# Kernel tuning notes

Measured on AMD Instinct MI355X. Metric: run time of the kernel, lower is better.

## Reference

```python
import jax, jax.numpy as jnp
import numpy as np

F_DIM = 128


def setup_inputs() -> dict:
    key = jax.random.key(0)
    ks = jax.random.split(key, 10)
    n_atoms = 50000
    n_edges = 500000
    F = F_DIM
    q = jax.random.normal(ks[0], (n_atoms, 1, F), dtype=jnp.float32)
    mu = jax.random.normal(ks[1], (n_atoms, 3, F), dtype=jnp.float32)
    Wij = jax.random.normal(ks[2], (n_edges, 1, 3 * F), dtype=jnp.float32)
    dir_ij = jax.random.normal(ks[3], (n_edges, 3), dtype=jnp.float32)
    idx_i = jax.random.randint(ks[4], (n_edges,), 0, n_atoms, dtype=jnp.int32)
    idx_j = jax.random.randint(ks[5], (n_edges,), 0, n_atoms, dtype=jnp.int32)
    # interatomic_context_net params: Dense(F,F,silu) -> Dense(F,3F)
    s1 = 1.0 / np.sqrt(F)
    W1 = jax.random.uniform(ks[6], (F, F), jnp.float32, -s1, s1)
    b1 = jax.random.uniform(ks[7], (F,), jnp.float32, -s1, s1)
    W2 = jax.random.uniform(ks[8], (F, 3 * F), jnp.float32, -s1, s1)
    b2 = jax.random.uniform(ks[9], (3 * F,), jnp.float32, -s1, s1)
    return {"q": q, "mu": mu, "Wij": Wij, "dir_ij": dir_ij,
            "W1": W1, "b1": b1, "W2": W2, "b2": b2,
            "idx_i": idx_i, "idx_j": idx_j, "n_atoms": n_atoms}


def reference(q, mu, Wij, dir_ij, W1, b1, W2, b2, idx_i, idx_j, n_atoms):
    F = F_DIM
    # context MLP on per-atom scalar features: [n_atoms, 1, 3F]
    h = jax.nn.silu(jnp.einsum('aif,fg->aig', q, W1) + b1)
    x = jnp.einsum('aif,fg->aig', h, W2) + b2
    # gather along edges
    xj = x[idx_j]          # [E, 1, 3F]
    muj = mu[idx_j]        # [E, 3, F]
    xw = Wij * xj          # [E, 1, 3F]
    dq, dmuR, dmumu = jnp.split(xw, 3, axis=-1)  # each [E, 1, F]
    dq_atom = jax.ops.segment_sum(dq, idx_i, num_segments=n_atoms)  # [n_atoms,1,F]
    dmu = dmuR * dir_ij[..., None] + dmumu * muj                    # [E,3,F]
    dmu_atom = jax.ops.segment_sum(dmu, idx_i, num_segments=n_atoms)
    return (q + dq_atom, mu + dmu_atom)
```

## Files before the change

### kernel.cpp

```cpp
#include <hip/hip_runtime.h>

typedef unsigned short u16;
typedef unsigned int   u32;

#define F 128
#define F3 384
#define TA 32
#define PAD 36

__device__ __forceinline__ float bf2f(u16 v) {
    union { u32 u; float f; } c; c.u = ((u32)v) << 16; return c.f;
}
__device__ __forceinline__ u16 f2bf(float f) {
    union { float fv; u32 u; } c; c.fv = f;
    u32 u = c.u;
    return (u16)((u + 0x7fffu + ((u >> 16) & 1u)) >> 16);
}

template<bool BF> __device__ __forceinline__ float LD(const void* p, size_t i) {
    return BF ? bf2f(((const u16*)p)[i]) : ((const float*)p)[i];
}
template<bool BF> __device__ __forceinline__ void ST(void* p, size_t i, float v) {
    if (BF) ((u16*)p)[i] = f2bf(v); else ((float*)p)[i] = v;
}
template<bool BF> __device__ __forceinline__ float2 LD2(const void* p, size_t i) {
    if (BF) {
        u32 v = *(const u32*)((const u16*)p + i);
        float2 r; r.x = bf2f((u16)(v & 0xffff)); r.y = bf2f((u16)(v >> 16)); return r;
    }
    return *(const float2*)((const float*)p + i);
}
template<bool BF> __device__ __forceinline__ void ST2(void* p, size_t i, float2 v) {
    if (BF) { *(u32*)((u16*)p + i) = ((u32)f2bf(v.y) << 16) | f2bf(v.x); }
    else    { *(float2*)((float*)p + i) = v; }
}
__device__ __forceinline__ float2 LD2bf(const u16* p, size_t i) {
    u32 v = *(const u32*)(p + i);
    float2 r; r.x = bf2f((u16)(v & 0xffff)); r.y = bf2f((u16)(v >> 16)); return r;
}
template<bool BF> __device__ __forceinline__ float4 LD4(const void* p, size_t i) {
    if (BF) {
        uint2 v = *(const uint2*)((const u16*)p + i);
        float4 r;
        r.x = bf2f((u16)(v.x & 0xffff)); r.y = bf2f((u16)(v.x >> 16));
        r.z = bf2f((u16)(v.y & 0xffff)); r.w = bf2f((u16)(v.y >> 16));
        return r;
    }
    return *(const float4*)((const float*)p + i);
}

__global__ __launch_bounds__(256) void detect_kernel(const void* q, int* flag) {
    __shared__ int cnt;
    if (threadIdx.x == 0) cnt = 0;
    __syncthreads();
    const u16* p = (const u16*)q;
    int c = 0;
    for (int i = threadIdx.x; i < 1024; i += 256) {
        u16 v = p[2 * i];
        int e = (v >> 7) & 0xFF;
        if (e >= 100 && e <= 150) c++;
    }
    atomicAdd(&cnt, c);
    __syncthreads();
    if (threadIdx.x == 0) *flag = (cnt > 512) ? 1 : 0;
}

template<bool BF>
__device__ void mlp_body(const void* q, const void* W1, const void* b1,
                         const void* W2, const void* b2,
                         u16* __restrict__ xc, u16* __restrict__ hbuf,
                         int cb, int mode, int n_atoms)
{
    __shared__ float qT[F][PAD];
    __shared__ float hT[F][PAD];

    const int tid = threadIdx.x;
    const int a0  = blockIdx.x * TA;
    const int c4  = (tid & 31) * 4;
    const int r4  = (tid >> 5) * 4;

    if (mode == 2) {
        for (int i = tid; i < TA * F / 8; i += 256) {
            int a = i >> 4, f0 = (i & 15) * 8;
            float4 v0, v1;
            if (a0 + a < n_atoms) {
                v0 = LD4<true>(hbuf, (size_t)(a0 + a) * F + f0);
                v1 = LD4<true>(hbuf, (size_t)(a0 + a) * F + f0 + 4);
            } else { v0 = v1 = make_float4(0, 0, 0, 0); }
            hT[f0 + 0][a] = v0.x; hT[f0 + 1][a] = v0.y; hT[f0 + 2][a] = v0.z; hT[f0 + 3][a] = v0.w;
            hT[f0 + 4][a] = v1.x; hT[f0 + 5][a] = v1.y; hT[f0 + 6][a] = v1.z; hT[f0 + 7][a] = v1.w;
        }
        __syncthreads();
    } else {
        for (int i = tid; i < TA * F / 8; i += 256) {
            int a = i >> 4, f0 = (i & 15) * 8;
            float4 v0, v1;
            if (a0 + a < n_atoms) {
                v0 = LD4<BF>(q, (size_t)(a0 + a) * F + f0);
                v1 = LD4<BF>(q, (size_t)(a0 + a) * F + f0 + 4);
            } else { v0 = v1 = make_float4(0, 0, 0, 0); }
            qT[f0 + 0][a] = v0.x; qT[f0 + 1][a] = v0.y; qT[f0 + 2][a] = v0.z; qT[f0 + 3][a] = v0.w;
            qT[f0 + 4][a] = v1.x; qT[f0 + 5][a] = v1.y; qT[f0 + 6][a] = v1.z; qT[f0 + 7][a] = v1.w;
        }
        __syncthreads();

        float acc[4][4];
#pragma unroll
        for (int rr = 0; rr < 4; ++rr)
#pragma unroll
            for (int cc = 0; cc < 4; ++cc) acc[rr][cc] = 0.0f;

        for (int f = 0; f < F; ++f) {
            float4 qv = *(const float4*)&qT[f][r4];
            float4 w  = LD4<BF>(W1, (size_t)f * F + c4);
            float qa[4] = {qv.x, qv.y, qv.z, qv.w};
            float wa[4] = {w.x, w.y, w.z, w.w};
#pragma unroll
            for (int rr = 0; rr < 4; ++rr)
#pragma unroll
                for (int cc = 0; cc < 4; ++cc)
                    acc[rr][cc] += qa[rr] * wa[cc];
        }
        float hv[4][4];
#pragma unroll
        for (int cc = 0; cc < 4; ++cc) {
            float bb = LD<BF>(b1, c4 + cc);
#pragma unroll
            for (int rr = 0; rr < 4; ++rr) {
                float h = acc[rr][cc] + bb;
                float s = h / (1.0f + __expf(-h));
                hv[rr][cc] = s;
                hT[c4 + cc][r4 + rr] = s;
            }
        }
        if (mode == 1) {
#pragma unroll
            for (int rr = 0; rr < 4; ++rr) {
                int ga = a0 + r4 + rr;
                if (ga < n_atoms) {
                    *(u32*)(hbuf + (size_t)ga * F + c4)     = ((u32)f2bf(hv[rr][1]) << 16) | f2bf(hv[rr][0]);
                    *(u32*)(hbuf + (size_t)ga * F + c4 + 2) = ((u32)f2bf(hv[rr][3]) << 16) | f2bf(hv[rr][2]);
                }
            }
        }
        __syncthreads();
    }

    float acc[4][4];
#pragma unroll
    for (int rr = 0; rr < 4; ++rr)
#pragma unroll
        for (int cc = 0; cc < 4; ++cc) acc[rr][cc] = 0.0f;

    for (int f = 0; f < F; ++f) {
        float4 hv = *(const float4*)&hT[f][r4];
        float4 w  = LD4<BF>(W2, (size_t)f * F3 + cb * F + c4);
        float ha[4] = {hv.x, hv.y, hv.z, hv.w};
        float wa[4] = {w.x, w.y, w.z, w.w};
#pragma unroll
        for (int rr = 0; rr < 4; ++rr)
#pragma unroll
            for (int cc = 0; cc < 4; ++cc)
                acc[rr][cc] += ha[rr] * wa[cc];
    }
    float bb[4];
#pragma unroll
    for (int cc = 0; cc < 4; ++cc) bb[cc] = LD<BF>(b2, cb * F + c4 + cc);
#pragma unroll
    for (int rr = 0; rr < 4; ++rr) {
        int ga = a0 + r4 + rr;
        if (ga < n_atoms) {
            float x0 = acc[rr][0] + bb[0], x1 = acc[rr][1] + bb[1];
            float x2 = acc[rr][2] + bb[2], x3 = acc[rr][3] + bb[3];
            *(u32*)(xc + (size_t)ga * F + c4)     = ((u32)f2bf(x1) << 16) | f2bf(x0);
            *(u32*)(xc + (size_t)ga * F + c4 + 2) = ((u32)f2bf(x3) << 16) | f2bf(x2);
        }
    }
}

__global__ __launch_bounds__(256) void mlp_kernel(
    const void* q, const void* W1, const void* b1, const void* W2, const void* b2,
    u16* xc, u16* hbuf, int cb, int mode, int n_atoms, const int* flag)
{
    if (*flag) mlp_body<true >(q, W1, b1, W2, b2, xc, hbuf, cb, mode, n_atoms);
    else       mlp_body<false>(q, W1, b1, W2, b2, xc, hbuf, cb, mode, n_atoms);
}

__global__ __launch_bounds__(256) void count_kernel(
    const int* __restrict__ idx_i, int* __restrict__ counts, int E)
{
    int e = blockIdx.x * 256 + threadIdx.x;
    if (e < E) atomicAdd(&counts[idx_i[e]], 1);
}

__global__ __launch_bounds__(1024) void scan_kernel(
    const int* __restrict__ counts, int* __restrict__ offsets, int n)
{
    __shared__ int buf[1024];
    __shared__ int carryS;
    const int t = threadIdx.x;
    if (t == 0) carryS = 0;
    __syncthreads();

    for (int base = 0; base < n; base += 8192) {
        int idx0 = base + t * 8;
        int c[8];
#pragma unroll
        for (int r = 0; r < 8; ++r) c[r] = (idx0 + r < n) ? counts[idx0 + r] : 0;
        int s = 0;
#pragma unroll
        for (int r = 0; r < 8; ++r) s += c[r];
        buf[t] = s;
        __syncthreads();
        for (int off = 1; off < 1024; off <<= 1) {
            int add = (t >= off) ? buf[t - off] : 0;
            __syncthreads();
            buf[t] += add;
            __syncthreads();
        }
        int run = carryS + buf[t] - s;
#pragma unroll
        for (int r = 0; r < 8; ++r) {
            if (idx0 + r < n) offsets[idx0 + r] = run;
            run += c[r];
        }
        __syncthreads();
        if (t == 0) carryS += buf[1023];
        __syncthreads();
    }
    if (t == 0) offsets[n] = carryS;
}

__global__ __launch_bounds__(256) void scatter_kernel(
    const int* __restrict__ idx_i, const int* __restrict__ offsets,
    int* __restrict__ cursor, int* __restrict__ perm, int E)
{
    int e = blockIdx.x * 256 + threadIdx.x;
    if (e < E) {
        int i = idx_i[e];
        int pos = offsets[i] + atomicAdd(&cursor[i], 1);
        perm[pos] = e;
    }
}

template<bool BF>
__device__ void gq_body(const void* q, const void* Wij, const u16* __restrict__ xc,
                        const int* __restrict__ idx_j, const int* __restrict__ offsets,
                        const int* __restrict__ perm, void* out, int n_atoms, int E)
{
    int a    = blockIdx.x * 4 + (threadIdx.x >> 6);
    int lane = threadIdx.x & 63;
    if (a >= n_atoms) return;
    const size_t fo = 2 * lane;

    float2 s = LD2<BF>(q, (size_t)a * F + fo);
    int k0 = offsets[a], k1 = offsets[a + 1];
    for (int kb = k0; kb < k1; kb += 64) {
        int cnt = k1 - kb; if (cnt > 64) cnt = 64;
        int e_r = 0, j_r = 0;
        if (lane < cnt) {
            e_r = perm[kb + lane]; if ((unsigned)e_r >= (unsigned)E) e_r = 0;
            j_r = idx_j[e_r];      if ((unsigned)j_r >= (unsigned)n_atoms) j_r = 0;
        }
        for (int c = 0; c < cnt; ++c) {
            int e = __shfl(e_r, c, 64);
            int j = __shfl(j_r, c, 64);
            float2 w  = LD2<BF>(Wij, (size_t)e * F3 + fo);
            float2 xv = LD2bf(xc, (size_t)j * F + fo);
            s.x += w.x * xv.x;
            s.y += w.y * xv.y;
        }
    }
    ST2<BF>(out, (size_t)a * F + fo, s);
}

__global__ __launch_bounds__(256) void gather_q_kernel(
    const void* q, const void* Wij, const u16* xc, const int* idx_j,
    const int* offsets, const int* perm, void* out, int n_atoms, int E, const int* flag)
{
    if (*flag) gq_body<true >(q, Wij, xc, idx_j, offsets, perm, out, n_atoms, E);
    else       gq_body<false>(q, Wij, xc, idx_j, offsets, perm, out, n_atoms, E);
}

template<bool BF, int MODE>
__device__ void gmu_body(const void* mu, const void* Wij, const void* dir,
                         const u16* __restrict__ xc, const int* __restrict__ idx_j,
                         const int* __restrict__ offsets, const int* __restrict__ perm,
                         void* out, int n_atoms, int E)
{
    int a    = blockIdx.x * 4 + (threadIdx.x >> 6);
    int lane = threadIdx.x & 63;
    if (a >= n_atoms) return;
    const size_t fo = 2 * lane;
    const size_t ob = (size_t)n_atoms * F;

    float2 s0, s1, s2;
    if (MODE == 1) {
        s0 = LD2<BF>(mu, (size_t)a * F3 + fo);
        s1 = LD2<BF>(mu, (size_t)a * F3 + 128 + fo);
        s2 = LD2<BF>(mu, (size_t)a * F3 + 256 + fo);
    } else {
        s0 = LD2<BF>(out, ob + (size_t)a * F3 + fo);
        s1 = LD2<BF>(out, ob + (size_t)a * F3 + 128 + fo);
        s2 = LD2<BF>(out, ob + (size_t)a * F3 + 256 + fo);
    }

    const int wofs = (MODE == 1) ? 128 : 256;
    int k0 = offsets[a], k1 = offsets[a + 1];
    for (int kb = k0; kb < k1; kb += 64) {
        int cnt = k1 - kb; if (cnt > 64) cnt = 64;
        int e_r = 0, j_r = 0;
        if (lane < cnt) {
            e_r = perm[kb + lane]; if ((unsigned)e_r >= (unsigned)E) e_r = 0;
            j_r = idx_j[e_r];      if ((unsigned)j_r >= (unsigned)n_atoms) j_r = 0;
        }
        for (int c = 0; c < cnt; ++c) {
            int e = __shfl(e_r, c, 64);
            int j = __shfl(j_r, c, 64);
            float2 w  = LD2<BF>(Wij, (size_t)e * F3 + wofs + fo);
            float2 xv = LD2bf(xc, (size_t)j * F + fo);
            float wx0 = w.x * xv.x, wx1 = w.y * xv.y;
            if (MODE == 1) {
                float d0 = LD<BF>(dir, (size_t)e * 3 + 0);
                float d1 = LD<BF>(dir, (size_t)e * 3 + 1);
                float d2 = LD<BF>(dir, (size_t)e * 3 + 2);
                s0.x += wx0 * d0; s0.y += wx1 * d0;
                s1.x += wx0 * d1; s1.y += wx1 * d1;
                s2.x += wx0 * d2; s2.y += wx1 * d2;
            } else {
                float2 m0 = LD2<BF>(mu, (size_t)j * F3 + fo);
                float2 m1 = LD2<BF>(mu, (size_t)j * F3 + 128 + fo);
                float2 m2 = LD2<BF>(mu, (size_t)j * F3 + 256 + fo);
                s0.x += wx0 * m0.x; s0.y += wx1 * m0.y;
                s1.x += wx0 * m1.x; s1.y += wx1 * m1.y;
                s2.x += wx0 * m2.x; s2.y += wx1 * m2.y;
            }
        }
    }
    ST2<BF>(out, ob + (size_t)a * F3 + fo,       s0);
    ST2<BF>(out, ob + (size_t)a * F3 + 128 + fo, s1);
    ST2<BF>(out, ob + (size_t)a * F3 + 256 + fo, s2);
}

__global__ __launch_bounds__(256) void gather_mu_kernel(
    const void* mu, const void* Wij, const void* dir, const u16* xc,
    const int* idx_j, const int* offsets, const int* perm, void* out,
    int n_atoms, int E, int mode, const int* flag)
{
    if (*flag) {
        if (mode == 1) gmu_body<true, 1>(mu, Wij, dir, xc, idx_j, offsets, perm, out, n_atoms, E);
        else           gmu_body<true, 2>(mu, Wij, dir, xc, idx_j, offsets, perm, out, n_atoms, E);
    } else {
        if (mode == 1) gmu_body<false, 1>(mu, Wij, dir, xc, idx_j, offsets, perm, out, n_atoms, E);
        else           gmu_body<false, 2>(mu, Wij, dir, xc, idx_j, offsets, perm, out, n_atoms, E);
    }
}

extern "C" void kernel_launch(void* const* d_in, const int* in_sizes, int n_in,
                              void* d_out, int out_size, void* d_ws, size_t ws_size,
                              hipStream_t stream)
{
    const void* q   = d_in[0];
    const void* mu  = d_in[1];
    const void* Wij = d_in[2];
    const void* dir = d_in[3];
    const void* W1  = d_in[4];
    const void* b1  = d_in[5];
    const void* W2  = d_in[6];
    const void* b2  = d_in[7];
    const int* idx_i = (const int*)d_in[8];
    const int* idx_j = (const int*)d_in[9];

    const int n_atoms = in_sizes[0] / F;
    const int E       = in_sizes[8];

    u16* xc      = (u16*)d_ws;
    int* flag    = (int*)(xc + (size_t)n_atoms * F);
    int* counts  = flag + 4;
    int* cursor  = counts + n_atoms;
    int* offsets = cursor + n_atoms;
    int* perm    = offsets + n_atoms + 1;
    u16* hbuf    = (u16*)(perm + E);
    size_t need_h = (size_t)((char*)(hbuf + (size_t)n_atoms * F) - (char*)d_ws);
    const bool useH = (ws_size >= need_h);

    detect_kernel<<<1, 256, 0, stream>>>(q, flag);

    hipMemsetAsync(counts, 0, (size_t)2 * n_atoms * sizeof(int), stream);
    int eBlocks = (E + 255) / 256;
    count_kernel<<<eBlocks, 256, 0, stream>>>(idx_i, counts, E);
    scan_kernel<<<1, 1024, 0, stream>>>(counts, offsets, n_atoms);
    scatter_kernel<<<eBlocks, 256, 0, stream>>>(idx_i, offsets, cursor, perm, E);

    int mlpBlocks = (n_atoms + TA - 1) / TA;
    int gBlocks   = (n_atoms + 3) / 4;

    mlp_kernel<<<mlpBlocks, 256, 0, stream>>>(q, W1, b1, W2, b2, xc, hbuf, 0,
                                              useH ? 1 : 0, n_atoms, flag);
    gather_q_kernel<<<gBlocks, 256, 0, stream>>>(q, Wij, xc, idx_j, offsets, perm,
                                                 d_out, n_atoms, E, flag);
    mlp_kernel<<<mlpBlocks, 256, 0, stream>>>(q, W1, b1, W2, b2, xc, hbuf, 1,
                                              useH ? 2 : 0, n_atoms, flag);
    gather_mu_kernel<<<gBlocks, 256, 0, stream>>>(mu, Wij, dir, xc, idx_j, offsets, perm,
                                                  d_out, n_atoms, E, 1, flag);
    mlp_kernel<<<mlpBlocks, 256, 0, stream>>>(q, W1, b1, W2, b2, xc, hbuf, 2,
                                              useH ? 2 : 0, n_atoms, flag);
    gather_mu_kernel<<<gBlocks, 256, 0, stream>>>(mu, Wij, dir, xc, idx_j, offsets, perm,
                                                  d_out, n_atoms, E, 2, flag);
}
```

Measured before the change: 682.0 us.

## Fuse MLP into one pass and merge q/mu gathers into one edge kernel

Adds a path, used when the workspace is large enough, that computes all three output chunks of the context MLP in one kernel into a full bf16 x buffer. It converts mu to bf16 once, then runs a single CSR gather kernel that accumulates dq and all three dmu components per edge. This replaces three MLP launches and three gather passes that each re-read the edge indices, Wij and neighbour rows. The scan kernel is also reworked to a single pass with per-thread contiguous chunks. The trade-off is a larger workspace, lower mu precision from the bf16 copy, and more registers in the fused gather.

```diff
diff --git a/kernel.cpp b/kernel.cpp
--- a/kernel.cpp
+++ b/kernel.cpp
@@ -63,6 +63,125 @@
     atomicAdd(&cnt, c);
     __syncthreads();
     if (threadIdx.x == 0) *flag = (cnt > 512) ? 1 : 0;
+}
+
+template<bool BF>
+__device__ void convmu_body(const void* mu, u16* dst, size_t n) {
+    size_t i = ((size_t)blockIdx.x * 256 + threadIdx.x) * 8;
+    if (i >= n) return;
+    if (BF) {
+        *(uint4*)(dst + i) = *(const uint4*)((const u16*)mu + i);
+    } else {
+        float4 a = *(const float4*)((const float*)mu + i);
+        float4 b = *(const float4*)((const float*)mu + i + 4);
+        uint4 o;
+        o.x = ((u32)f2bf(a.y) << 16) | f2bf(a.x);
+        o.y = ((u32)f2bf(a.w) << 16) | f2bf(a.z);
+        o.z = ((u32)f2bf(b.y) << 16) | f2bf(b.x);
+        o.w = ((u32)f2bf(b.w) << 16) | f2bf(b.z);
+        *(uint4*)(dst + i) = o;
+    }
+}
+__global__ __launch_bounds__(256) void convmu_kernel(const void* mu, u16* dst,
+                                                     size_t n, const int* flag) {
+    if (*flag) convmu_body<true >(mu, dst, n);
+    else       convmu_body<false>(mu, dst, n);
+}
+
+template<bool BF>
+__device__ void mlpfull_body(const void* q, const void* W1, const void* b1,
+                             const void* W2, const void* b2,
+                             u16* __restrict__ xcf, int n_atoms)
+{
+    __shared__ float qT[F][PAD];
+    __shared__ float hT[F][PAD];
+
+    const int tid = threadIdx.x;
+    const int a0  = blockIdx.x * TA;
+    const int c4  = (tid & 31) * 4;
+    const int r4  = (tid >> 5) * 4;
+
+    for (int i = tid; i < TA * F / 8; i += 256) {
+        int a = i >> 4, f0 = (i & 15) * 8;
+        float4 v0, v1;
+        if (a0 + a < n_atoms) {
+            v0 = LD4<BF>(q, (size_t)(a0 + a) * F + f0);
+            v1 = LD4<BF>(q, (size_t)(a0 + a) * F + f0 + 4);
+        } else { v0 = v1 = make_float4(0, 0, 0, 0); }
+        qT[f0 + 0][a] = v0.x; qT[f0 + 1][a] = v0.y; qT[f0 + 2][a] = v0.z; qT[f0 + 3][a] = v0.w;
+        qT[f0 + 4][a] = v1.x; qT[f0 + 5][a] = v1.y; qT[f0 + 6][a] = v1.z; qT[f0 + 7][a] = v1.w;
+    }
+    __syncthreads();
+
+    {
+        float acc[4][4];
+#pragma unroll
+        for (int rr = 0; rr < 4; ++rr)
+#pragma unroll
+            for (int cc = 0; cc < 4; ++cc) acc[rr][cc] = 0.0f;
+
+        for (int f = 0; f < F; ++f) {
+            float4 qv = *(const float4*)&qT[f][r4];
+            float4 w  = LD4<BF>(W1, (size_t)f * F + c4);
+            float qa[4] = {qv.x, qv.y, qv.z, qv.w};
+            float wa[4] = {w.x, w.y, w.z, w.w};
+#pragma unroll
+            for (int rr = 0; rr < 4; ++rr)
+#pragma unroll
+                for (int cc = 0; cc < 4; ++cc)
+                    acc[rr][cc] += qa[rr] * wa[cc];
+        }
+#pragma unroll
+        for (int cc = 0; cc < 4; ++cc) {
+            float bb = LD<BF>(b1, c4 + cc);
+#pragma unroll
+            for (int rr = 0; rr < 4; ++rr) {
+                float h = acc[rr][cc] + bb;
+                hT[c4 + cc][r4 + rr] = h / (1.0f + __expf(-h));
+            }
+        }
+    }
+    __syncthreads();
+
+    for (int cb = 0; cb < 3; ++cb) {
+        float acc[4][4];
+#pragma unroll
+        for (int rr = 0; rr < 4; ++rr)
+#pragma unroll
+            for (int cc = 0; cc < 4; ++cc) acc[rr][cc] = 0.0f;
+
+        for (int f = 0; f < F; ++f) {
+            float4 hv = *(const float4*)&hT[f][r4];
+            float4 w  = LD4<BF>(W2, (size_t)f * F3 + cb * F + c4);
+            float ha[4] = {hv.x, hv.y, hv.z, hv.w};
+            float wa[4] = {w.x, w.y, w.z, w.w};
+#pragma unroll
+            for (int rr = 0; rr < 4; ++rr)
+#pragma unroll
+                for (int cc = 0; cc < 4; ++cc)
+                    acc[rr][cc] += ha[rr] * wa[cc];
+        }
+        float bb[4];
+#pragma unroll
+        for (int cc = 0; cc < 4; ++cc) bb[cc] = LD<BF>(b2, cb * F + c4 + cc);
+#pragma unroll
+        for (int rr = 0; rr < 4; ++rr) {
+            int ga = a0 + r4 + rr;
+            if (ga < n_atoms) {
+                uint2 o;
+                o.x = ((u32)f2bf(acc[rr][1] + bb[1]) << 16) | f2bf(acc[rr][0] + bb[0]);
+                o.y = ((u32)f2bf(acc[rr][3] + bb[3]) << 16) | f2bf(acc[rr][2] + bb[2]);
+                *(uint2*)(xcf + (size_t)ga * F3 + cb * F + c4) = o;
+            }
+        }
+    }
+}
+__global__ __launch_bounds__(256) void mlpfull_kernel(
+    const void* q, const void* W1, const void* b1, const void* W2, const void* b2,
+    u16* xcf, int n_atoms, const int* flag)
+{
+    if (*flag) mlpfull_body<true >(q, W1, b1, W2, b2, xcf, n_atoms);
+    else       mlpfull_body<false>(q, W1, b1, W2, b2, xcf, n_atoms);
 }
 
 template<bool BF>
@@ -170,14 +289,11 @@
     for (int rr = 0; rr < 4; ++rr) {
         int ga = a0 + r4 + rr;
         if (ga < n_atoms) {
-            float x0 = acc[rr][0] + bb[0], x1 = acc[rr][1] + bb[1];
-            float x2 = acc[rr][2] + bb[2], x3 = acc[rr][3] + bb[3];
-            *(u32*)(xc + (size_t)ga * F + c4)     = ((u32)f2bf(x1) << 16) | f2bf(x0);
-            *(u32*)(xc + (size_t)ga * F + c4 + 2) = ((u32)f2bf(x3) << 16) | f2bf(x2);
-        }
-    }
-}
-
+            *(u32*)(xc + (size_t)ga * F + c4)     = ((u32)f2bf(acc[rr][1] + bb[1]) << 16) | f2bf(acc[rr][0] + bb[0]);
+            *(u32*)(xc + (size_t)ga * F + c4 + 2) = ((u32)f2bf(acc[rr][3] + bb[3]) << 16) | f2bf(acc[rr][2] + bb[2]);
+        }
+    }
+}
 __global__ __launch_bounds__(256) void mlp_kernel(
     const void* q, const void* W1, const void* b1, const void* W2, const void* b2,
     u16* xc, u16* hbuf, int cb, int mode, int n_atoms, const int* flag)
@@ -197,38 +313,28 @@
     const int* __restrict__ counts, int* __restrict__ offsets, int n)
 {
     __shared__ int buf[1024];
-    __shared__ int carryS;
     const int t = threadIdx.x;
-    if (t == 0) carryS = 0;
+    const int m = (n + 1023) >> 10;
+    const int i0 = t * m;
+    int s = 0;
+    for (int r = 0; r < m; ++r) {
+        int i = i0 + r;
+        if (i < n) s += counts[i];
+    }
+    buf[t] = s;
     __syncthreads();
-
-    for (int base = 0; base < n; base += 8192) {
-        int idx0 = base + t * 8;
-        int c[8];
-#pragma unroll
-        for (int r = 0; r < 8; ++r) c[r] = (idx0 + r < n) ? counts[idx0 + r] : 0;
-        int s = 0;
-#pragma unroll
-        for (int r = 0; r < 8; ++r) s += c[r];
-        buf[t] = s;
+    for (int off = 1; off < 1024; off <<= 1) {
+        int add = (t >= off) ? buf[t - off] : 0;
         __syncthreads();
-        for (int off = 1; off < 1024; off <<= 1) {
-            int add = (t >= off) ? buf[t - off] : 0;
-            __syncthreads();
-            buf[t] += add;
-            __syncthreads();
-        }
-        int run = carryS + buf[t] - s;
-#pragma unroll
-        for (int r = 0; r < 8; ++r) {
-            if (idx0 + r < n) offsets[idx0 + r] = run;
-            run += c[r];
-        }
+        buf[t] += add;
         __syncthreads();
-        if (t == 0) carryS += buf[1023];
-        __syncthreads();
-    }
-    if (t == 0) offsets[n] = carryS;
+    }
+    int run = buf[t] - s;
+    for (int r = 0; r < m; ++r) {
+        int i = i0 + r;
+        if (i < n) { offsets[i] = run; run += counts[i]; }
+    }
+    if (t == 1023) offsets[n] = buf[1023];
 }
 
 __global__ __launch_bounds__(256) void scatter_kernel(
@@ -241,6 +347,75 @@
         int pos = offsets[i] + atomicAdd(&cursor[i], 1);
         perm[pos] = e;
     }
+}
+
+template<bool BF>
+__device__ void gfused_body(const void* q, const void* mu, const void* Wij,
+                            const void* dir, const u16* __restrict__ xcf,
+                            const u16* __restrict__ mubf,
+                            const int* __restrict__ idx_j,
+                            const int* __restrict__ offsets,
+                            const int* __restrict__ perm,
+                            void* out, int n_atoms, int E)
+{
+    int a    = blockIdx.x * 4 + (threadIdx.x >> 6);
+    int lane = threadIdx.x & 63;
+    if (a >= n_atoms) return;
+    const size_t fo = 2 * lane;
+    const size_t ob = (size_t)n_atoms * F;
+
+    float2 sq = LD2<BF>(q, (size_t)a * F + fo);
+    float2 s0 = LD2<BF>(mu, (size_t)a * F3 + fo);
+    float2 s1 = LD2<BF>(mu, (size_t)a * F3 + 128 + fo);
+    float2 s2 = LD2<BF>(mu, (size_t)a * F3 + 256 + fo);
+
+    int k0 = offsets[a], k1 = offsets[a + 1];
+    for (int kb = k0; kb < k1; kb += 64) {
+        int cnt = k1 - kb; if (cnt > 64) cnt = 64;
+        int e_r = 0, j_r = 0;
+        if (lane < cnt) {
+            e_r = perm[kb + lane]; if ((unsigned)e_r >= (unsigned)E) e_r = 0;
+            j_r = idx_j[e_r];      if ((unsigned)j_r >= (unsigned)n_atoms) j_r = 0;
+        }
+#pragma unroll 2
+        for (int c = 0; c < cnt; ++c) {
+            int e = __shfl(e_r, c, 64);
+            int j = __shfl(j_r, c, 64);
+            const size_t wb = (size_t)e * F3;
+            const size_t jb = (size_t)j * F3;
+            float2 wq = LD2<BF>(Wij, wb + fo);
+            float2 wR = LD2<BF>(Wij, wb + 128 + fo);
+            float2 wm = LD2<BF>(Wij, wb + 256 + fo);
+            float2 xq = LD2bf(xcf, jb + fo);
+            float2 xR = LD2bf(xcf, jb + 128 + fo);
+            float2 xm = LD2bf(xcf, jb + 256 + fo);
+            float2 m0 = LD2bf(mubf, jb + fo);
+            float2 m1 = LD2bf(mubf, jb + 128 + fo);
+            float2 m2 = LD2bf(mubf, jb + 256 + fo);
+            float d0 = LD<BF>(dir, (size_t)e * 3 + 0);
+            float d1 = LD<BF>(dir, (size_t)e * 3 + 1);
+            float d2 = LD<BF>(dir, (size_t)e * 3 + 2);
+
+            sq.x += wq.x * xq.x;           sq.y += wq.y * xq.y;
+            float tR0 = wR.x * xR.x,  tR1 = wR.y * xR.y;
+            float tm0 = wm.x * xm.x,  tm1 = wm.y * xm.y;
+            s0.x += tR0 * d0 + tm0 * m0.x; s0.y += tR1 * d0 + tm1 * m0.y;
+            s1.x += tR0 * d1 + tm0 * m1.x; s1.y += tR1 * d1 + tm1 * m1.y;
+            s2.x += tR0 * d2 + tm0 * m2.x; s2.y += tR1 * d2 + tm1 * m2.y;
+        }
+    }
+    ST2<BF>(out, (size_t)a * F + fo, sq);
+    ST2<BF>(out, ob + (size_t)a * F3 + fo,       s0);
+    ST2<BF>(out, ob + (size_t)a * F3 + 128 + fo, s1);
+    ST2<BF>(out, ob + (size_t)a * F3 + 256 + fo, s2);
+}
+__global__ __launch_bounds__(256) void gfused_kernel(
+    const void* q, const void* mu, const void* Wij, const void* dir,
+    const u16* xcf, const u16* mubf, const int* idx_j, const int* offsets,
+    const int* perm, void* out, int n_atoms, int E, const int* flag)
+{
+    if (*flag) gfused_body<true >(q, mu, Wij, dir, xcf, mubf, idx_j, offsets, perm, out, n_atoms, E);
+    else       gfused_body<false>(q, mu, Wij, dir, xcf, mubf, idx_j, offsets, perm, out, n_atoms, E);
 }
 
 template<bool BF>
@@ -273,7 +448,6 @@
     }
     ST2<BF>(out, (size_t)a * F + fo, s);
 }
-
 __global__ __launch_bounds__(256) void gather_q_kernel(
     const void* q, const void* Wij, const u16* xc, const int* idx_j,
     const int* offsets, const int* perm, void* out, int n_atoms, int E, const int* flag)
@@ -341,7 +515,6 @@
     ST2<BF>(out, ob + (size_t)a * F3 + 128 + fo, s1);
     ST2<BF>(out, ob + (size_t)a * F3 + 256 + fo, s2);
 }
-
 __global__ __launch_bounds__(256) void gather_mu_kernel(
     const void* mu, const void* Wij, const void* dir, const u16* xc,
     const int* idx_j, const int* offsets, const int* perm, void* out,
@@ -373,6 +546,37 @@
 
     const int n_atoms = in_sizes[0] / F;
     const int E       = in_sizes[8];
+    const int eBlocks = (E + 255) / 256;
+    const int gBlocks = (n_atoms + 3) / 4;
+    const int mlpBlocks = (n_atoms + TA - 1) / TA;
+
+    {
+        u16* xcf     = (u16*)d_ws;
+        u16* mubf    = xcf + (size_t)n_atoms * F3;
+        int* flag    = (int*)(mubf + (size_t)n_atoms * F3);
+        int* counts  = flag + 4;
+        int* cursor  = counts + n_atoms;
+        int* offsets = cursor + n_atoms;
+        int* perm    = offsets + n_atoms + 1;
+        size_t need  = (size_t)((char*)(perm + E) - (char*)d_ws);
+
+        if (ws_size >= need) {
+            detect_kernel<<<1, 256, 0, stream>>>(q, flag);
+            hipMemsetAsync(counts, 0, (size_t)2 * n_atoms * sizeof(int), stream);
+            count_kernel<<<eBlocks, 256, 0, stream>>>(idx_i, counts, E);
+            scan_kernel<<<1, 1024, 0, stream>>>(counts, offsets, n_atoms);
+            scatter_kernel<<<eBlocks, 256, 0, stream>>>(idx_i, offsets, cursor, perm, E);
+
+            size_t nmu = (size_t)n_atoms * F3;
+            convmu_kernel<<<(int)((nmu / 8 + 255) / 256), 256, 0, stream>>>(mu, mubf, nmu, flag);
+            mlpfull_kernel<<<mlpBlocks, 256, 0, stream>>>(q, W1, b1, W2, b2, xcf, n_atoms, flag);
+
+            gfused_kernel<<<gBlocks, 256, 0, stream>>>(q, mu, Wij, dir, xcf, mubf,
+                                                       idx_j, offsets, perm, d_out,
+                                                       n_atoms, E, flag);
+            return;
+        }
+    }
 
     u16* xc      = (u16*)d_ws;
     int* flag    = (int*)(xc + (size_t)n_atoms * F);
@@ -385,15 +589,10 @@
     const bool useH = (ws_size >= need_h);
 
     detect_kernel<<<1, 256, 0, stream>>>(q, flag);
-
     hipMemsetAsync(counts, 0, (size_t)2 * n_atoms * sizeof(int), stream);
-    int eBlocks = (E + 255) / 256;
     count_kernel<<<eBlocks, 256, 0, stream>>>(idx_i, counts, E);
     scan_kernel<<<1, 1024, 0, stream>>>(counts, offsets, n_atoms);
     scatter_kernel<<<eBlocks, 256, 0, stream>>>(idx_i, offsets, cursor, perm, E);
-
-    int mlpBlocks = (n_atoms + TA - 1) / TA;
-    int gBlocks   = (n_atoms + 3) / 4;
 
     mlp_kernel<<<mlpBlocks, 256, 0, stream>>>(q, W1, b1, W2, b2, xc, hbuf, 0,
                                               useH ? 1 : 0, n_atoms, flag);
```

Result: faster. 605.0 us (-11.3%).

## Fuse three gather passes into one with interleaved per-atom x/mu rows

Applied to the files above, without the earlier changes.

Replaces the three separate MLP+gather passes with a single MLP kernel that computes all three 128-wide output chunks and one fused gather kernel that reads each edge's full Wij row once. The x values and a bf16 copy of mu are interleaved into one 768-element row per atom, so each neighbor needs one contiguous fetch. The sorted edge list is packed into int4 records carrying e, j and bf16 direction, and Wij loads and output stores use nontemporal hints. This cuts repeated reads of Wij, idx_j and mu along with extra launches. In exchange it uses a larger workspace, quantizes mu and dir to bf16 in the gather, and keeps more registers live in the MLP.

```diff
diff --git a/kernel.cpp b/kernel.cpp
--- a/kernel.cpp
+++ b/kernel.cpp
@@ -2,11 +2,13 @@
 
 typedef unsigned short u16;
 typedef unsigned int   u32;
+typedef unsigned long long u64;
 
 #define F 128
 #define F3 384
 #define TA 32
 #define PAD 36
+#define ROW 768
 
 __device__ __forceinline__ float bf2f(u16 v) {
     union { u32 u; float f; } c; c.u = ((u32)v) << 16; return c.f;
@@ -16,12 +18,18 @@
     u32 u = c.u;
     return (u16)((u + 0x7fffu + ((u >> 16) & 1u)) >> 16);
 }
+__device__ __forceinline__ float u2f(u32 v) {
+    union { u32 u; float f; } c; c.u = v; return c.f;
+}
+__device__ __forceinline__ u32 f2u(float v) {
+    union { float f; u32 u; } c; c.f = v; return c.u;
+}
+__device__ __forceinline__ u32 pk(float a, float b) {
+    return ((u32)f2bf(b) << 16) | f2bf(a);
+}
 
 template<bool BF> __device__ __forceinline__ float LD(const void* p, size_t i) {
     return BF ? bf2f(((const u16*)p)[i]) : ((const float*)p)[i];
-}
-template<bool BF> __device__ __forceinline__ void ST(void* p, size_t i, float v) {
-    if (BF) ((u16*)p)[i] = f2bf(v); else ((float*)p)[i] = v;
 }
 template<bool BF> __device__ __forceinline__ float2 LD2(const void* p, size_t i) {
     if (BF) {
@@ -31,7 +39,7 @@
     return *(const float2*)((const float*)p + i);
 }
 template<bool BF> __device__ __forceinline__ void ST2(void* p, size_t i, float2 v) {
-    if (BF) { *(u32*)((u16*)p + i) = ((u32)f2bf(v.y) << 16) | f2bf(v.x); }
+    if (BF) { *(u32*)((u16*)p + i) = pk(v.x, v.y); }
     else    { *(float2*)((float*)p + i) = v; }
 }
 __device__ __forceinline__ float2 LD2bf(const u16* p, size_t i) {
@@ -48,6 +56,24 @@
     }
     return *(const float4*)((const float*)p + i);
 }
+template<bool BF> __device__ __forceinline__ float2 NTLD2(const void* p, size_t i) {
+    if (BF) {
+        u32 v = __builtin_nontemporal_load((const u32*)((const u16*)p + i));
+        float2 r; r.x = bf2f((u16)(v & 0xffff)); r.y = bf2f((u16)(v >> 16)); return r;
+    } else {
+        u64 v = __builtin_nontemporal_load((const u64*)((const float*)p + i));
+        float2 r; r.x = u2f((u32)v); r.y = u2f((u32)(v >> 32)); return r;
+    }
+}
+template<bool BF> __device__ __forceinline__ void NTST2(void* p, size_t i, float2 v) {
+    if (BF) {
+        u32 o = pk(v.x, v.y);
+        __builtin_nontemporal_store(o, (u32*)((u16*)p + i));
+    } else {
+        u64 o = ((u64)f2u(v.y) << 32) | f2u(v.x);
+        __builtin_nontemporal_store(o, (u64*)((float*)p + i));
+    }
+}
 
 __global__ __launch_bounds__(256) void detect_kernel(const void* q, int* flag) {
     __shared__ int cnt;
@@ -66,10 +92,27 @@
 }
 
 template<bool BF>
-__device__ void mlp_body(const void* q, const void* W1, const void* b1,
-                         const void* W2, const void* b2,
-                         u16* __restrict__ xc, u16* __restrict__ hbuf,
-                         int cb, int mode, int n_atoms)
+__device__ void mu12_body(const void* mu, u16* xm12, int n_atoms) {
+    int a = blockIdx.x * 4 + (threadIdx.x >> 6);
+    int p = threadIdx.x & 63;
+    if (a >= n_atoms) return;
+    float2 m0 = LD2<BF>(mu, (size_t)a * F3 + 2 * p);
+    float2 m1 = LD2<BF>(mu, (size_t)a * F3 + 128 + 2 * p);
+    float2 m2 = LD2<BF>(mu, (size_t)a * F3 + 256 + 2 * p);
+    u16* base = xm12 + (size_t)a * ROW + p * 12;
+    *(u32*)(base + 6) = pk(m0.x, m0.y);
+    *(uint2*)(base + 8) = make_uint2(pk(m1.x, m1.y), pk(m2.x, m2.y));
+}
+__global__ __launch_bounds__(256) void mu12_kernel(const void* mu, u16* xm12,
+                                                   int n_atoms, const int* flag) {
+    if (*flag) mu12_body<true >(mu, xm12, n_atoms);
+    else       mu12_body<false>(mu, xm12, n_atoms);
+}
+
+template<bool BF>
+__device__ void mlpfull_body(const void* q, const void* W1, const void* b1,
+                             const void* W2, const void* b2,
+                             u16* __restrict__ xm12, int n_atoms)
 {
     __shared__ float qT[F][PAD];
     __shared__ float hT[F][PAD];
@@ -79,31 +122,19 @@
     const int c4  = (tid & 31) * 4;
     const int r4  = (tid >> 5) * 4;
 
-    if (mode == 2) {
-        for (int i = tid; i < TA * F / 8; i += 256) {
-            int a = i >> 4, f0 = (i & 15) * 8;
-            float4 v0, v1;
-            if (a0 + a < n_atoms) {
-                v0 = LD4<true>(hbuf, (size_t)(a0 + a) * F + f0);
-                v1 = LD4<true>(hbuf, (size_t)(a0 + a) * F + f0 + 4);
-            } else { v0 = v1 = make_float4(0, 0, 0, 0); }
-            hT[f0 + 0][a] = v0.x; hT[f0 + 1][a] = v0.y; hT[f0 + 2][a] = v0.z; hT[f0 + 3][a] = v0.w;
-            hT[f0 + 4][a] = v1.x; hT[f0 + 5][a] = v1.y; hT[f0 + 6][a] = v1.z; hT[f0 + 7][a] = v1.w;
-        }
-        __syncthreads();
-    } else {
-        for (int i = tid; i < TA * F / 8; i += 256) {
-            int a = i >> 4, f0 = (i & 15) * 8;
-            float4 v0, v1;
-            if (a0 + a < n_atoms) {
-                v0 = LD4<BF>(q, (size_t)(a0 + a) * F + f0);
-                v1 = LD4<BF>(q, (size_t)(a0 + a) * F + f0 + 4);
-            } else { v0 = v1 = make_float4(0, 0, 0, 0); }
-            qT[f0 + 0][a] = v0.x; qT[f0 + 1][a] = v0.y; qT[f0 + 2][a] = v0.z; qT[f0 + 3][a] = v0.w;
-            qT[f0 + 4][a] = v1.x; qT[f0 + 5][a] = v1.y; qT[f0 + 6][a] = v1.z; qT[f0 + 7][a] = v1.w;
-        }
-        __syncthreads();
-
+    for (int i = tid; i < TA * F / 8; i += 256) {
+        int a = i >> 4, f0 = (i & 15) * 8;
+        float4 v0, v1;
+        if (a0 + a < n_atoms) {
+            v0 = LD4<BF>(q, (size_t)(a0 + a) * F + f0);
+            v1 = LD4<BF>(q, (size_t)(a0 + a) * F + f0 + 4);
+        } else { v0 = v1 = make_float4(0, 0, 0, 0); }
+        qT[f0 + 0][a] = v0.x; qT[f0 + 1][a] = v0.y; qT[f0 + 2][a] = v0.z; qT[f0 + 3][a] = v0.w;
+        qT[f0 + 4][a] = v1.x; qT[f0 + 5][a] = v1.y; qT[f0 + 6][a] = v1.z; qT[f0 + 7][a] = v1.w;
+    }
+    __syncthreads();
+
+    {
         float acc[4][4];
 #pragma unroll
         for (int rr = 0; rr < 4; ++rr)
@@ -121,69 +152,68 @@
                 for (int cc = 0; cc < 4; ++cc)
                     acc[rr][cc] += qa[rr] * wa[cc];
         }
-        float hv[4][4];
 #pragma unroll
         for (int cc = 0; cc < 4; ++cc) {
             float bb = LD<BF>(b1, c4 + cc);
 #pragma unroll
             for (int rr = 0; rr < 4; ++rr) {
                 float h = acc[rr][cc] + bb;
-                float s = h / (1.0f + __expf(-h));
-                hv[rr][cc] = s;
-                hT[c4 + cc][r4 + rr] = s;
+                hT[c4 + cc][r4 + rr] = h / (1.0f + __expf(-h));
             }
         }
-        if (mode == 1) {
-#pragma unroll
-            for (int rr = 0; rr < 4; ++rr) {
-                int ga = a0 + r4 + rr;
-                if (ga < n_atoms) {
-                    *(u32*)(hbuf + (size_t)ga * F + c4)     = ((u32)f2bf(hv[rr][1]) << 16) | f2bf(hv[rr][0]);
-                    *(u32*)(hbuf + (size_t)ga * F + c4 + 2) = ((u32)f2bf(hv[rr][3]) << 16) | f2bf(hv[rr][2]);
-                }
-            }
-        }
-        __syncthreads();
-    }
-
-    float acc[4][4];
-#pragma unroll
-    for (int rr = 0; rr < 4; ++rr)
-#pragma unroll
-        for (int cc = 0; cc < 4; ++cc) acc[rr][cc] = 0.0f;
-
-    for (int f = 0; f < F; ++f) {
-        float4 hv = *(const float4*)&hT[f][r4];
-        float4 w  = LD4<BF>(W2, (size_t)f * F3 + cb * F + c4);
-        float ha[4] = {hv.x, hv.y, hv.z, hv.w};
-        float wa[4] = {w.x, w.y, w.z, w.w};
+    }
+    __syncthreads();
+
+    float xout[4][4][3];
+#pragma unroll
+    for (int cb = 0; cb < 3; ++cb) {
+        float acc[4][4];
 #pragma unroll
         for (int rr = 0; rr < 4; ++rr)
 #pragma unroll
-            for (int cc = 0; cc < 4; ++cc)
-                acc[rr][cc] += ha[rr] * wa[cc];
-    }
-    float bb[4];
-#pragma unroll
-    for (int cc = 0; cc < 4; ++cc) bb[cc] = LD<BF>(b2, cb * F + c4 + cc);
+            for (int cc = 0; cc < 4; ++cc) acc[rr][cc] = 0.0f;
+
+        for (int f = 0; f < F; ++f) {
+            float4 hv = *(const float4*)&hT[f][r4];
+            float4 w  = LD4<BF>(W2, (size_t)f * F3 + cb * F + c4);
+            float ha[4] = {hv.x, hv.y, hv.z, hv.w};
+            float wa[4] = {w.x, w.y, w.z, w.w};
+#pragma unroll
+            for (int rr = 0; rr < 4; ++rr)
+#pragma unroll
+                for (int cc = 0; cc < 4; ++cc)
+                    acc[rr][cc] += ha[rr] * wa[cc];
+        }
+#pragma unroll
+        for (int cc = 0; cc < 4; ++cc) {
+            float bb = LD<BF>(b2, cb * F + c4 + cc);
+#pragma unroll
+            for (int rr = 0; rr < 4; ++rr)
+                xout[rr][cc][cb] = acc[rr][cc] + bb;
+        }
+    }
 #pragma unroll
     for (int rr = 0; rr < 4; ++rr) {
         int ga = a0 + r4 + rr;
         if (ga < n_atoms) {
-            float x0 = acc[rr][0] + bb[0], x1 = acc[rr][1] + bb[1];
-            float x2 = acc[rr][2] + bb[2], x3 = acc[rr][3] + bb[3];
-            *(u32*)(xc + (size_t)ga * F + c4)     = ((u32)f2bf(x1) << 16) | f2bf(x0);
-            *(u32*)(xc + (size_t)ga * F + c4 + 2) = ((u32)f2bf(x3) << 16) | f2bf(x2);
-        }
-    }
-}
-
-__global__ __launch_bounds__(256) void mlp_kernel(
+            int p0 = c4 >> 1;
+            u16* b0 = xm12 + (size_t)ga * ROW + p0 * 12;
+            *(uint2*)(b0) = make_uint2(pk(xout[rr][0][0], xout[rr][1][0]),
+                                       pk(xout[rr][0][1], xout[rr][1][1]));
+            *(u32*)(b0 + 4) = pk(xout[rr][0][2], xout[rr][1][2]);
+            u16* b1p = b0 + 12;
+            *(uint2*)(b1p) = make_uint2(pk(xout[rr][2][0], xout[rr][3][0]),
+                                        pk(xout[rr][2][1], xout[rr][3][1]));
+            *(u32*)(b1p + 4) = pk(xout[rr][2][2], xout[rr][3][2]);
+        }
+    }
+}
+__global__ __launch_bounds__(256) void mlpfull_kernel(
     const void* q, const void* W1, const void* b1, const void* W2, const void* b2,
-    u16* xc, u16* hbuf, int cb, int mode, int n_atoms, const int* flag)
-{
-    if (*flag) mlp_body<true >(q, W1, b1, W2, b2, xc, hbuf, cb, mode, n_atoms);
-    else       mlp_body<false>(q, W1, b1, W2, b2, xc, hbuf, cb, mode, n_atoms);
+    u16* xm12, int n_atoms, const int* flag)
+{
+    if (*flag) mlpfull_body<true >(q, W1, b1, W2, b2, xm12, n_atoms);
+    else       mlpfull_body<false>(q, W1, b1, W2, b2, xm12, n_atoms);
 }
 
 __global__ __launch_bounds__(256) void count_kernel(
@@ -197,96 +227,64 @@
     const int* __restrict__ counts, int* __restrict__ offsets, int n)
 {
     __shared__ int buf[1024];
-    __shared__ int carryS;
     const int t = threadIdx.x;
-    if (t == 0) carryS = 0;
-    __syncthreads();
-
-    for (int base = 0; base < n; base += 8192) {
-        int idx0 = base + t * 8;
-        int c[8];
-#pragma unroll
-        for (int r = 0; r < 8; ++r) c[r] = (idx0 + r < n) ? counts[idx0 + r] : 0;
-        int s = 0;
-#pragma unroll
-        for (int r = 0; r < 8; ++r) s += c[r];
-        buf[t] = s;
+    const int m = (n + 1023) >> 10;
+    const int i0 = t * m;
+    int s = 0;
+    for (int r = 0; r < m; ++r) {
+        int i = i0 + r;
+        if (i < n) s += counts[i];
+    }
+    buf[t] = s;
+    __syncthreads();
+    for (int off = 1; off < 1024; off <<= 1) {
+        int add = (t >= off) ? buf[t - off] : 0;
         __syncthreads();
-        for (int off = 1; off < 1024; off <<= 1) {
-            int add = (t >= off) ? buf[t - off] : 0;
-            __syncthreads();
-            buf[t] += add;
-            __syncthreads();
-        }
-        int run = carryS + buf[t] - s;
-#pragma unroll
-        for (int r = 0; r < 8; ++r) {
-            if (idx0 + r < n) offsets[idx0 + r] = run;
-            run += c[r];
-        }
+        buf[t] += add;
         __syncthreads();
-        if (t == 0) carryS += buf[1023];
-        __syncthreads();
-    }
-    if (t == 0) offsets[n] = carryS;
-}
-
-__global__ __launch_bounds__(256) void scatter_kernel(
-    const int* __restrict__ idx_i, const int* __restrict__ offsets,
-    int* __restrict__ cursor, int* __restrict__ perm, int E)
+    }
+    int run = buf[t] - s;
+    for (int r = 0; r < m; ++r) {
+        int i = i0 + r;
+        if (i < n) { offsets[i] = run; run += counts[i]; }
+    }
+    if (t == 1023) offsets[n] = buf[1023];
+}
+
+template<bool BF>
+__device__ void scatter_body(const int* __restrict__ idx_i, const int* __restrict__ idx_j,
+                             const void* __restrict__ dir, const int* __restrict__ offsets,
+                             int* __restrict__ cursor, int4* __restrict__ ej4, int E)
 {
     int e = blockIdx.x * 256 + threadIdx.x;
     if (e < E) {
         int i = idx_i[e];
         int pos = offsets[i] + atomicAdd(&cursor[i], 1);
-        perm[pos] = e;
-    }
+        float d0 = LD<BF>(dir, (size_t)e * 3 + 0);
+        float d1 = LD<BF>(dir, (size_t)e * 3 + 1);
+        float d2 = LD<BF>(dir, (size_t)e * 3 + 2);
+        int4 v;
+        v.x = e;
+        v.y = idx_j[e];
+        v.z = (int)pk(d0, d1);
+        v.w = (int)(u32)f2bf(d2);
+        ej4[pos] = v;
+    }
+}
+__global__ __launch_bounds__(256) void scatter_kernel(
+    const int* idx_i, const int* idx_j, const void* dir, const int* offsets,
+    int* cursor, int4* ej4, int E, const int* flag)
+{
+    if (*flag) scatter_body<true >(idx_i, idx_j, dir, offsets, cursor, ej4, E);
+    else       scatter_body<false>(idx_i, idx_j, dir, offsets, cursor, ej4, E);
 }
 
 template<bool BF>
-__device__ void gq_body(const void* q, const void* Wij, const u16* __restrict__ xc,
-                        const int* __restrict__ idx_j, const int* __restrict__ offsets,
-                        const int* __restrict__ perm, void* out, int n_atoms, int E)
-{
-    int a    = blockIdx.x * 4 + (threadIdx.x >> 6);
-    int lane = threadIdx.x & 63;
-    if (a >= n_atoms) return;
-    const size_t fo = 2 * lane;
-
-    float2 s = LD2<BF>(q, (size_t)a * F + fo);
-    int k0 = offsets[a], k1 = offsets[a + 1];
-    for (int kb = k0; kb < k1; kb += 64) {
-        int cnt = k1 - kb; if (cnt > 64) cnt = 64;
-        int e_r = 0, j_r = 0;
-        if (lane < cnt) {
-            e_r = perm[kb + lane]; if ((unsigned)e_r >= (unsigned)E) e_r = 0;
-            j_r = idx_j[e_r];      if ((unsigned)j_r >= (unsigned)n_atoms) j_r = 0;
-        }
-        for (int c = 0; c < cnt; ++c) {
-            int e = __shfl(e_r, c, 64);
-            int j = __shfl(j_r, c, 64);
-            float2 w  = LD2<BF>(Wij, (size_t)e * F3 + fo);
-            float2 xv = LD2bf(xc, (size_t)j * F + fo);
-            s.x += w.x * xv.x;
-            s.y += w.y * xv.y;
-        }
-    }
-    ST2<BF>(out, (size_t)a * F + fo, s);
-}
-
-__global__ __launch_bounds__(256) void gather_q_kernel(
-    const void* q, const void* Wij, const u16* xc, const int* idx_j,
-    const int* offsets, const int* perm, void* out, int n_atoms, int E, const int* flag)
-{
-    if (*flag) gq_body<true >(q, Wij, xc, idx_j, offsets, perm, out, n_atoms, E);
-    else       gq_body<false>(q, Wij, xc, idx_j, offsets, perm, out, n_atoms, E);
-}
-
-template<bool BF, int MODE>
-__device__ void gmu_body(const void* mu, const void* Wij, const void* dir,
-                         const u16* __restrict__ xc, const int* __restrict__ idx_j,
-                         const int* __restrict__ offsets, const int* __restrict__ perm,
-                         void* out, int n_atoms, int E)
+__device__ void gfused_body(const void* q, const void* mu, const void* Wij,
+                            const u16* __restrict__ xm12,
+                            const int4* __restrict__ ej4,
+                            const int* __restrict__ offsets,
+                            void* out, int n_atoms, int E)
 {
     int a    = blockIdx.x * 4 + (threadIdx.x >> 6);
     int lane = threadIdx.x & 63;
@@ -294,66 +292,67 @@
     const size_t fo = 2 * lane;
     const size_t ob = (size_t)n_atoms * F;
 
-    float2 s0, s1, s2;
-    if (MODE == 1) {
-        s0 = LD2<BF>(mu, (size_t)a * F3 + fo);
-        s1 = LD2<BF>(mu, (size_t)a * F3 + 128 + fo);
-        s2 = LD2<BF>(mu, (size_t)a * F3 + 256 + fo);
-    } else {
-        s0 = LD2<BF>(out, ob + (size_t)a * F3 + fo);
-        s1 = LD2<BF>(out, ob + (size_t)a * F3 + 128 + fo);
-        s2 = LD2<BF>(out, ob + (size_t)a * F3 + 256 + fo);
-    }
-
-    const int wofs = (MODE == 1) ? 128 : 256;
+    float2 sq = LD2<BF>(q, (size_t)a * F + fo);
+    float2 s0 = LD2<BF>(mu, (size_t)a * F3 + fo);
+    float2 s1 = LD2<BF>(mu, (size_t)a * F3 + 128 + fo);
+    float2 s2 = LD2<BF>(mu, (size_t)a * F3 + 256 + fo);
+
     int k0 = offsets[a], k1 = offsets[a + 1];
     for (int kb = k0; kb < k1; kb += 64) {
         int cnt = k1 - kb; if (cnt > 64) cnt = 64;
-        int e_r = 0, j_r = 0;
+        int e_r = 0, j_r = 0, d01_r = 0, d2_r = 0;
         if (lane < cnt) {
-            e_r = perm[kb + lane]; if ((unsigned)e_r >= (unsigned)E) e_r = 0;
-            j_r = idx_j[e_r];      if ((unsigned)j_r >= (unsigned)n_atoms) j_r = 0;
-        }
+            int4 t = ej4[kb + lane];
+            e_r = t.x; if ((unsigned)e_r >= (unsigned)E) e_r = 0;
+            j_r = t.y; if ((unsigned)j_r >= (unsigned)n_atoms) j_r = 0;
+            d01_r = t.z; d2_r = t.w;
+        }
+#pragma unroll 4
         for (int c = 0; c < cnt; ++c) {
-            int e = __shfl(e_r, c, 64);
-            int j = __shfl(j_r, c, 64);
-            float2 w  = LD2<BF>(Wij, (size_t)e * F3 + wofs + fo);
-            float2 xv = LD2bf(xc, (size_t)j * F + fo);
-            float wx0 = w.x * xv.x, wx1 = w.y * xv.y;
-            if (MODE == 1) {
-                float d0 = LD<BF>(dir, (size_t)e * 3 + 0);
-                float d1 = LD<BF>(dir, (size_t)e * 3 + 1);
-                float d2 = LD<BF>(dir, (size_t)e * 3 + 2);
-                s0.x += wx0 * d0; s0.y += wx1 * d0;
-                s1.x += wx0 * d1; s1.y += wx1 * d1;
-                s2.x += wx0 * d2; s2.y += wx1 * d2;
-            } else {
-                float2 m0 = LD2<BF>(mu, (size_t)j * F3 + fo);
-                float2 m1 = LD2<BF>(mu, (size_t)j * F3 + 128 + fo);
-                float2 m2 = LD2<BF>(mu, (size_t)j * F3 + 256 + fo);
-                s0.x += wx0 * m0.x; s0.y += wx1 * m0.y;
-                s1.x += wx0 * m1.x; s1.y += wx1 * m1.y;
-                s2.x += wx0 * m2.x; s2.y += wx1 * m2.y;
-            }
-        }
-    }
-    ST2<BF>(out, ob + (size_t)a * F3 + fo,       s0);
-    ST2<BF>(out, ob + (size_t)a * F3 + 128 + fo, s1);
-    ST2<BF>(out, ob + (size_t)a * F3 + 256 + fo, s2);
-}
-
-__global__ __launch_bounds__(256) void gather_mu_kernel(
-    const void* mu, const void* Wij, const void* dir, const u16* xc,
-    const int* idx_j, const int* offsets, const int* perm, void* out,
-    int n_atoms, int E, int mode, const int* flag)
-{
-    if (*flag) {
-        if (mode == 1) gmu_body<true, 1>(mu, Wij, dir, xc, idx_j, offsets, perm, out, n_atoms, E);
-        else           gmu_body<true, 2>(mu, Wij, dir, xc, idx_j, offsets, perm, out, n_atoms, E);
-    } else {
-        if (mode == 1) gmu_body<false, 1>(mu, Wij, dir, xc, idx_j, offsets, perm, out, n_atoms, E);
-        else           gmu_body<false, 2>(mu, Wij, dir, xc, idx_j, offsets, perm, out, n_atoms, E);
-    }
+            int e   = __shfl(e_r, c, 64);
+            int j   = __shfl(j_r, c, 64);
+            int d01 = __shfl(d01_r, c, 64);
+            int d2i = __shfl(d2_r, c, 64);
+            float d0 = bf2f((u16)((u32)d01 & 0xffff));
+            float d1 = bf2f((u16)((u32)d01 >> 16));
+            float d2 = bf2f((u16)((u32)d2i & 0xffff));
+
+            float2 wq = NTLD2<BF>(Wij, (size_t)e * F3 + fo);
+            float2 wR = NTLD2<BF>(Wij, (size_t)e * F3 + 128 + fo);
+            float2 wm = NTLD2<BF>(Wij, (size_t)e * F3 + 256 + fo);
+
+            const u16* row = xm12 + (size_t)j * ROW + lane * 12;
+            uint2 v0 = *(const uint2*)(row);
+            uint2 v1 = *(const uint2*)(row + 4);
+            uint2 v2 = *(const uint2*)(row + 8);
+
+            float xq0 = bf2f((u16)(v0.x & 0xffff)), xq1 = bf2f((u16)(v0.x >> 16));
+            float xR0 = bf2f((u16)(v0.y & 0xffff)), xR1 = bf2f((u16)(v0.y >> 16));
+            float xm0 = bf2f((u16)(v1.x & 0xffff)), xm1 = bf2f((u16)(v1.x >> 16));
+            float m00 = bf2f((u16)(v1.y & 0xffff)), m01 = bf2f((u16)(v1.y >> 16));
+            float m10 = bf2f((u16)(v2.x & 0xffff)), m11 = bf2f((u16)(v2.x >> 16));
+            float m20 = bf2f((u16)(v2.y & 0xffff)), m21 = bf2f((u16)(v2.y >> 16));
+
+            sq.x += wq.x * xq0;  sq.y += wq.y * xq1;
+            float tR0 = wR.x * xR0, tR1 = wR.y * xR1;
+            float tm0 = wm.x * xm0, tm1 = wm.y * xm1;
+            s0.x += tR0 * d0 + tm0 * m00;  s0.y += tR1 * d0 + tm1 * m01;
+            s1.x += tR0 * d1 + tm0 * m10;  s1.y += tR1 * d1 + tm1 * m11;
+            s2.x += tR0 * d2 + tm0 * m20;  s2.y += tR1 * d2 + tm1 * m21;
+        }
+    }
+    NTST2<BF>(out, (size_t)a * F + fo, sq);
+    NTST2<BF>(out, ob + (size_t)a * F3 + fo,       s0);
+    NTST2<BF>(out, ob + (size_t)a * F3 + 128 + fo, s1);
+    NTST2<BF>(out, ob + (size_t)a * F3 + 256 + fo, s2);
+}
+__global__ __launch_bounds__(256) void gfused_kernel(
+    const void* q, const void* mu, const void* Wij,
+    const u16* xm12, const int4* ej4, const int* offsets,
+    void* out, int n_atoms, int E, const int* flag)
+{
+    if (*flag) gfused_body<true >(q, mu, Wij, xm12, ej4, offsets, out, n_atoms, E);
+    else       gfused_body<false>(q, mu, Wij, xm12, ej4, offsets, out, n_atoms, E);
 }
 
 extern "C" void kernel_launch(void* const* d_in, const int* in_sizes, int n_in,
@@ -373,38 +372,27 @@
 
     const int n_atoms = in_sizes[0] / F;
     const int E       = in_sizes[8];
-
-    u16* xc      = (u16*)d_ws;
-    int* flag    = (int*)(xc + (size_t)n_atoms * F);
-    int* counts  = flag + 4;
-    int* cursor  = counts + n_atoms;
-    int* offsets = cursor + n_atoms;
-    int* perm    = offsets + n_atoms + 1;
-    u16* hbuf    = (u16*)(perm + E);
-    size_t need_h = (size_t)((char*)(hbuf + (size_t)n_atoms * F) - (char*)d_ws);
-    const bool useH = (ws_size >= need_h);
+    const int eBlocks   = (E + 255) / 256;
+    const int gBlocks   = (n_atoms + 3) / 4;
+    const int mlpBlocks = (n_atoms + TA - 1) / TA;
+
+    u16*  xm12    = (u16*)d_ws;
+    int*  flag    = (int*)(xm12 + (size_t)n_atoms * ROW);
+    int*  counts  = flag + 4;
+    int*  cursor  = counts + n_atoms;
+    int*  offsets = cursor + n_atoms;
+    int4* ej4     = (int4*)(((size_t)(offsets + n_atoms + 1) + 15) & ~(size_t)15);
 
     detect_kernel<<<1, 256, 0, stream>>>(q, flag);
-
     hipMemsetAsync(counts, 0, (size_t)2 * n_atoms * sizeof(int), stream);
-    int eBlocks = (E + 255) / 256;
     count_kernel<<<eBlocks, 256, 0, stream>>>(idx_i, counts, E);
     scan_kernel<<<1, 1024, 0, stream>>>(counts, offsets, n_atoms);
-    scatter_kernel<<<eBlocks, 256, 0, stream>>>(idx_i, offsets, cursor, perm, E);
-
-    int mlpBlocks = (n_atoms + TA - 1) / TA;
-    int gBlocks   = (n_atoms + 3) / 4;
-
-    mlp_kernel<<<mlpBlocks, 256, 0, stream>>>(q, W1, b1, W2, b2, xc, hbuf, 0,
-                                              useH ? 1 : 0, n_atoms, flag);
-    gather_q_kernel<<<gBlocks, 256, 0, stream>>>(q, Wij, xc, idx_j, offsets, perm,
-                                                 d_out, n_atoms, E, flag);
-    mlp_kernel<<<mlpBlocks, 256, 0, stream>>>(q, W1, b1, W2, b2, xc, hbuf, 1,
-                                              useH ? 2 : 0, n_atoms, flag);
-    gather_mu_kernel<<<gBlocks, 256, 0, stream>>>(mu, Wij, dir, xc, idx_j, offsets, perm,
-                                                  d_out, n_atoms, E, 1, flag);
-    mlp_kernel<<<mlpBlocks, 256, 0, stream>>>(q, W1, b1, W2, b2, xc, hbuf, 2,
-                                              useH ? 2 : 0, n_atoms, flag);
-    gather_mu_kernel<<<gBlocks, 256, 0, stream>>>(mu, Wij, dir, xc, idx_j, offsets, perm,
-                                                  d_out, n_atoms, E, 2, flag);
-}
+    scatter_kernel<<<eBlocks, 256, 0, stream>>>(idx_i, idx_j, dir, offsets,
+                                                cursor, ej4, E, flag);
+
+    mu12_kernel<<<gBlocks, 256, 0, stream>>>(mu, xm12, n_atoms, flag);
+    mlpfull_kernel<<<mlpBlocks, 256, 0, stream>>>(q, W1, b1, W2, b2, xm12, n_atoms, flag);
+
+    gfused_kernel<<<gBlocks, 256, 0, stream>>>(q, mu, Wij, xm12, ej4, offsets,
+                                               d_out, n_atoms, E, flag);
+}
```

Result: faster. 586.1 us (-14.1%).
